# Performance work log

Measured on AMD Instinct MI355X. Metric: run time of the kernel, lower is better.

The kernel has to match this reference:

```python
import jax, jax.numpy as jnp
import numpy as np

L = 2        # layer_depth
H = 128      # rnn_size (== embedding dim)
V = 50257    # vocab_size
B = 100      # batch_size
T = 50       # seq_length


def setup_inputs() -> dict:
    key = jax.random.key(0)
    ks = jax.random.split(key, 8)
    inp = {
        'input_data': jax.random.randint(ks[0], (B, T), 0, V, dtype=jnp.int32),
        # embedding ~ U(-0.08, 0.08) as in the original
        'embedding': jax.random.uniform(ks[1], (V, H), jnp.float32, -0.08, 0.08),
        # per-layer GRU params; input dim == H for every layer
        'gate_k': jax.random.normal(ks[2], (L, 2 * H, 2 * H), jnp.float32) * 0.05,
        'gate_b': jnp.ones((L, 2 * H), jnp.float32),  # TF GRUCell gate bias init = 1.0
        'cand_k': jax.random.normal(ks[3], (L, 2 * H, H), jnp.float32) * 0.05,
        'cand_b': jnp.zeros((L, H), jnp.float32),
        'softmax_w': jax.random.normal(ks[4], (V, H), jnp.float32) * 0.05,
        'softmax_b': jnp.zeros((V,), jnp.float32),
    }
    return inp


def _gru_scan(x_bth, gate_k, gate_b, cand_k, cand_b):
    # x_bth: [B, T, H] embedded inputs. Stacked L-layer GRU, TF GRUCell math:
    #   r,u = sigmoid([x,h] @ Wg + bg);  c = tanh([x, r*h] @ Wc + bc)
    #   h' = u*h + (1-u)*c
    x_tbh = jnp.swapaxes(x_bth, 0, 1)  # [T, B, H]
    h0 = jnp.zeros((L, x_bth.shape[0], H), x_bth.dtype)

    def step(hs, x_t):
        inp = x_t
        new_hs = []
        for l in range(L):
            h = hs[l]
            g = jax.nn.sigmoid(jnp.concatenate([inp, h], -1) @ gate_k[l] + gate_b[l])
            r, u = g[:, :H], g[:, H:]
            c = jnp.tanh(jnp.concatenate([inp, r * h], -1) @ cand_k[l] + cand_b[l])
            h_new = u * h + (1.0 - u) * c
            new_hs.append(h_new)
            inp = h_new
        return jnp.stack(new_hs), inp

    final_state, out_tbh = jax.lax.scan(step, h0, x_tbh)
    return jnp.swapaxes(out_tbh, 0, 1), final_state  # [B, T, H], [L, B, H]


def reference(input_data, embedding, gate_k, gate_b, cand_k, cand_b, softmax_w, softmax_b):
    x = embedding[input_data]                                   # [B, T, H]
    out, _ = _gru_scan(x, gate_k, gate_b, cand_k, cand_b)       # [B, T, H]
    out = out.reshape(-1, H)                                    # [B*T, H]
    logits = out @ softmax_w.T + softmax_b                      # [B*T, V]
    probs = jax.nn.softmax(logits, axis=-1)
    return logits, probs
```

## Files before the change

### kernel.cpp

```cpp
#include <hip/hip_runtime.h>
#include <hip/hip_bf16.h>
#include <math.h>

#define GL 2
#define GH 128
#define GH2 256
#define GV 50257
#define GB 100
#define GT 50
#define GM 5000
#define NT 393
#define MT 40

typedef __attribute__((ext_vector_type(4))) float f32x4;
typedef __attribute__((ext_vector_type(8))) short bf16x8;

__global__ __launch_bounds__(1024) void gru_kernel(
    const int* __restrict__ tok,
    const float* __restrict__ emb,
    const float* __restrict__ gate_k,
    const float* __restrict__ gate_b,
    const float* __restrict__ cand_k,
    const float* __restrict__ cand_b,
    float* __restrict__ out)
{
    const int b = blockIdx.x;
    const int tid = threadIdx.x;

    __shared__ float xin[GH2];
    __shared__ float hs[2][GH];
    __shared__ float g[GH2];
    __shared__ float gpart[4][GH2];
    __shared__ float cpart[8][GH];

    if (tid < GH) { hs[0][tid] = 0.f; hs[1][tid] = 0.f; }
    __syncthreads();

    for (int t = 0; t < GT; ++t) {
        const int token = tok[b * GT + t];
        if (tid < GH) xin[tid] = emb[(size_t)token * GH + tid];

        for (int l = 0; l < GL; ++l) {
            if (tid >= GH && tid < GH2) xin[tid] = hs[l][tid - GH];
            __syncthreads();

            {
                const int j  = tid & 255;
                const int t4 = tid >> 8;
                const float* gcol = gate_k + (size_t)l * GH2 * GH2 + (size_t)(t4 * 64) * GH2 + j;
                const float* xv = xin + t4 * 64;
                float acc = 0.f;
                #pragma unroll 16
                for (int i = 0; i < 64; ++i) acc += xv[i] * gcol[(size_t)i * GH2];
                gpart[t4][j] = acc;
            }
            __syncthreads();
            if (tid < GH2) {
                float s = gpart[0][tid] + gpart[1][tid] + gpart[2][tid] + gpart[3][tid]
                        + gate_b[l * GH2 + tid];
                g[tid] = 1.f / (1.f + expf(-s));
            }
            __syncthreads();
            if (tid >= GH && tid < GH2) xin[tid] = g[tid - GH] * hs[l][tid - GH];
            __syncthreads();

            {
                const int j  = tid & 127;
                const int t8 = tid >> 7;
                const float* ccol = cand_k + (size_t)l * GH2 * GH + (size_t)(t8 * 32) * GH + j;
                const float* xv = xin + t8 * 32;
                float acc = 0.f;
                #pragma unroll 16
                for (int i = 0; i < 32; ++i) acc += xv[i] * ccol[(size_t)i * GH];
                cpart[t8][j] = acc;
            }
            __syncthreads();
            if (tid < GH) {
                float csum = 0.f;
                #pragma unroll
                for (int p = 0; p < 8; ++p) csum += cpart[p][tid];
                const float c = tanhf(csum + cand_b[l * GH + tid]);
                const float u = g[GH + tid];
                const float hn = u * hs[l][tid] + (1.f - u) * c;
                hs[l][tid] = hn;
                xin[tid] = hn;
                if (l == GL - 1) out[(size_t)(b * GT + t) * GH + tid] = hn;
            }
            __syncthreads();
        }
    }
}

__device__ __forceinline__ unsigned short f2bf(float x) {
    union { float f; unsigned u; } c; c.f = x;
    unsigned r = c.u + 0x7FFFu + ((c.u >> 16) & 1u);
    return (unsigned short)(r >> 16);
}
__device__ __forceinline__ float bf2f(unsigned short b) {
    union { unsigned u; float f; } c; c.u = ((unsigned)b) << 16; return c.f;
}

__global__ __launch_bounds__(256) void prep_kernel(
    const float* __restrict__ src, unsigned short* __restrict__ dst,
    int ntiles, int nrows)
{
    const int idx = blockIdx.x * 256 + threadIdx.x;
    if (idx >= ntiles * 4 * 128) return;
    const int r    = idx & 127;
    const int c    = idx >> 7;
    const int cs   = c & 3;
    const int tile = c >> 2;
    int row = tile * 128 + r; if (row > nrows - 1) row = nrows - 1;
    const float* s = src + (size_t)row * GH + (cs & 1) * 64;
    unsigned short* d = dst + (size_t)c * 8192 + r * 64;
    const bool lo = (cs >= 2);
    const int rx = r & 7;

    #pragma unroll
    for (int gq = 0; gq < 8; ++gq) {
        float x[8];
        *(float4*)(x)     = *(const float4*)(s + gq * 8);
        *(float4*)(x + 4) = *(const float4*)(s + gq * 8 + 4);
        unsigned u[4];
        #pragma unroll
        for (int q = 0; q < 4; ++q) {
            const float a0 = x[q * 2], a1 = x[q * 2 + 1];
            const unsigned short hi0 = f2bf(a0), hi1 = f2bf(a1);
            unsigned short h0, h1;
            if (lo) { h0 = f2bf(a0 - bf2f(hi0)); h1 = f2bf(a1 - bf2f(hi1)); }
            else    { h0 = hi0; h1 = hi1; }
            u[q] = (unsigned)h0 | ((unsigned)h1 << 16);
        }
        *(uint4*)(d + (size_t)((gq ^ rx) * 8)) = *(const uint4*)u;
    }
}

__global__ __launch_bounds__(256) void mfma_logits_kernel(
    const unsigned short* __restrict__ Ap, const unsigned short* __restrict__ Wp,
    const float* __restrict__ bias,
    float* __restrict__ logits, float* __restrict__ pmax, float* __restrict__ psum)
{
    __shared__ unsigned short ldsA[8192];
    __shared__ unsigned short ldsW[8192];
    __shared__ float sM[2][128];
    __shared__ float sS[2][128];

    const int bm  = blockIdx.x;
    const int bt  = blockIdx.y;
    const int tid = threadIdx.x;
    const int wid  = tid >> 6;
    const int lane = tid & 63;
    const int wm = wid >> 1, wn = wid & 1;
    const int l15 = lane & 15, l4 = lane >> 4;

    f32x4 acc[4][4];
    #pragma unroll
    for (int i = 0; i < 4; ++i)
        #pragma unroll
        for (int j = 0; j < 4; ++j) acc[i][j] = (f32x4){0.f, 0.f, 0.f, 0.f};

    #pragma unroll
    for (int s = 0; s < 6; ++s) {
        const int ac = (s < 2) ? s : (s < 4) ? (s - 2) : (s - 2);
        const int wc = (s < 4) ? s : (s - 4);
        const unsigned short* ga = Ap + (size_t)(bm * 4 + ac) * 8192 + wid * 2048 + lane * 8;
        const unsigned short* gw = Wp + (size_t)(bt * 4 + wc) * 8192 + wid * 2048 + lane * 8;
        #pragma unroll
        for (int i = 0; i < 4; ++i)
            __builtin_amdgcn_global_load_lds(
                (const __attribute__((address_space(1))) void*)(ga + i * 512),
                (__attribute__((address_space(3))) void*)(&ldsA[wid * 2048 + i * 512]), 16, 0, 0);
        #pragma unroll
        for (int i = 0; i < 4; ++i)
            __builtin_amdgcn_global_load_lds(
                (const __attribute__((address_space(1))) void*)(gw + i * 512),
                (__attribute__((address_space(3))) void*)(&ldsW[wid * 2048 + i * 512]), 16, 0, 0);
        __syncthreads();

        #pragma unroll
        for (int ks = 0; ks < 2; ++ks) {
            bf16x8 af[4], bf[4];
            #pragma unroll
            for (int mi = 0; mi < 4; ++mi) {
                const int row = wm * 64 + mi * 16 + l15;
                const int off = row * 64 + ((ks * 32 + l4 * 8) ^ ((row & 7) << 3));
                af[mi] = *(const bf16x8*)&ldsA[off];
            }
            #pragma unroll
            for (int nj = 0; nj < 4; ++nj) {
                const int row = wn * 64 + nj * 16 + l15;
                const int off = row * 64 + ((ks * 32 + l4 * 8) ^ ((row & 7) << 3));
                bf[nj] = *(const bf16x8*)&ldsW[off];
            }
            #pragma unroll
            for (int mi = 0; mi < 4; ++mi)
                #pragma unroll
                for (int nj = 0; nj < 4; ++nj)
                    acc[mi][nj] = __builtin_amdgcn_mfma_f32_16x16x32_bf16(
                        af[mi], bf[nj], acc[mi][nj], 0, 0, 0);
        }
        __syncthreads();
    }

    float bj[4]; bool nv[4];
    #pragma unroll
    for (int nj = 0; nj < 4; ++nj) {
        const int n = bt * 128 + wn * 64 + nj * 16 + l15;
        nv[nj] = (n < GV);
        bj[nj] = nv[nj] ? bias[n] : 0.f;
    }
    #pragma unroll
    for (int mi = 0; mi < 4; ++mi) {
        #pragma unroll
        for (int r = 0; r < 4; ++r) {
            const int rowb = wm * 64 + mi * 16 + l4 * 4 + r;
            const int m = bm * 128 + rowb;
            float v[4];
            #pragma unroll
            for (int nj = 0; nj < 4; ++nj) v[nj] = acc[mi][nj][r] + bj[nj];
            if (m < GM) {
                #pragma unroll
                for (int nj = 0; nj < 4; ++nj)
                    if (nv[nj])
                        logits[(size_t)m * GV + (bt * 128 + wn * 64 + nj * 16 + l15)] = v[nj];
            }
            float mx = -INFINITY;
            #pragma unroll
            for (int nj = 0; nj < 4; ++nj) if (nv[nj]) mx = fmaxf(mx, v[nj]);
            #pragma unroll
            for (int d = 1; d < 16; d <<= 1) mx = fmaxf(mx, __shfl_xor(mx, d));
            float se = 0.f;
            #pragma unroll
            for (int nj = 0; nj < 4; ++nj) if (nv[nj]) se += __expf(v[nj] - mx);
            #pragma unroll
            for (int d = 1; d < 16; d <<= 1) se += __shfl_xor(se, d);
            if (l15 == 0) { sM[wn][rowb] = mx; sS[wn][rowb] = se; }
        }
    }
    __syncthreads();
    if (tid < 128) {
        const int m = bm * 128 + tid;
        if (m < GM) {
            const float m0 = sM[0][tid], m1 = sM[1][tid];
            const float M = fmaxf(m0, m1);
            const float S = sS[0][tid] * __expf(m0 - M) + sS[1][tid] * __expf(m1 - M);
            pmax[(size_t)m * NT + bt] = M;
            psum[(size_t)m * NT + bt] = S;
        }
    }
}

__global__ __launch_bounds__(64) void reduce_kernel(
    const float* __restrict__ pmax, const float* __restrict__ psum,
    float* __restrict__ rowM, float* __restrict__ rowInvS)
{
    const int m = blockIdx.x;
    const int lane = threadIdx.x;
    float M = -INFINITY, S = 0.f;
    for (int t = lane; t < NT; t += 64) {
        const float m2 = pmax[(size_t)m * NT + t];
        const float s2 = psum[(size_t)m * NT + t];
        const float nM = fmaxf(M, m2);
        S = S * expf(M - nM) + s2 * expf(m2 - nM);
        M = nM;
    }
    #pragma unroll
    for (int d = 1; d < 64; d <<= 1) {
        const float m2 = __shfl_xor(M, d);
        const float s2 = __shfl_xor(S, d);
        const float nM = fmaxf(M, m2);
        S = S * expf(M - nM) + s2 * expf(m2 - nM);
        M = nM;
    }
    if (lane == 0) { rowM[m] = M; rowInvS[m] = 1.f / S; }
}

__global__ __launch_bounds__(256) void probs_kernel(
    const float* __restrict__ logits,
    const float* __restrict__ rowM, const float* __restrict__ rowInvS,
    float* __restrict__ probs)
{
    const float4* L4 = reinterpret_cast<const float4*>(logits);
    float4* P4 = reinterpret_cast<float4*>(probs);
    const int n4 = (int)(((long long)GM * GV) / 4);
    const int stride = gridDim.x * blockDim.x;
    for (int i = blockIdx.x * blockDim.x + threadIdx.x; i < n4; i += stride) {
        const float4 v = L4[i];
        const int base = i * 4;
        const int m0 = base / GV;
        const int m3 = (base + 3) / GV;
        float4 o;
        if (m0 == m3) {
            const float M = rowM[m0], Is = rowInvS[m0];
            o.x = __expf(v.x - M) * Is;
            o.y = __expf(v.y - M) * Is;
            o.z = __expf(v.z - M) * Is;
            o.w = __expf(v.w - M) * Is;
        } else {
            const int ma = base / GV, mb = (base + 1) / GV;
            const int mc = (base + 2) / GV, md = (base + 3) / GV;
            o.x = __expf(v.x - rowM[ma]) * rowInvS[ma];
            o.y = __expf(v.y - rowM[mb]) * rowInvS[mb];
            o.z = __expf(v.z - rowM[mc]) * rowInvS[mc];
            o.w = __expf(v.w - rowM[md]) * rowInvS[md];
        }
        P4[i] = o;
    }
}

extern "C" void kernel_launch(void* const* d_in, const int* in_sizes, int n_in,
                              void* d_out, int out_size, void* d_ws, size_t ws_size,
                              hipStream_t stream) {
    const int*   tok    = (const int*)d_in[0];
    const float* emb    = (const float*)d_in[1];
    const float* gate_k = (const float*)d_in[2];
    const float* gate_b = (const float*)d_in[3];
    const float* cand_k = (const float*)d_in[4];
    const float* cand_b = (const float*)d_in[5];
    const float* W      = (const float*)d_in[6];
    const float* bias   = (const float*)d_in[7];

    float* logits = (float*)d_out;
    float* probs  = logits + (size_t)GM * GV;

    float* ws = (float*)d_ws;
    float* gruout = ws;
    unsigned short* Ap = (unsigned short*)(gruout + 640000);
    unsigned short* Wp = Ap + (size_t)MT * 4 * 8192;
    float* pmax    = (float*)(Wp + (size_t)NT * 4 * 8192);
    float* psum    = pmax + (size_t)GM * NT;
    float* rowM    = psum + (size_t)GM * NT;
    float* rowInvS = rowM + GM;

    gru_kernel<<<GB, 1024, 0, stream>>>(tok, emb, gate_k, gate_b, cand_k, cand_b, gruout);

    prep_kernel<<<(MT * 4 * 128 + 255) / 256, 256, 0, stream>>>(gruout, Ap, MT, GM);
    prep_kernel<<<(NT * 4 * 128 + 255) / 256, 256, 0, stream>>>(W, Wp, NT, GV);

    dim3 g2(MT, NT);
    mfma_logits_kernel<<<g2, 256, 0, stream>>>(Ap, Wp, bias, logits, pmax, psum);

    reduce_kernel<<<GM, 64, 0, stream>>>(pmax, psum, rowM, rowInvS);

    probs_kernel<<<4096, 256, 0, stream>>>(logits, rowM, rowInvS, probs);
}
```

Baseline: 1.369 ms.

## Share each W tile across two M tiles in 512-thread logits blocks

The logits GEMM block now covers 256 rows with 8 waves and two A tiles in LDS that share one W tile, which halves the number of W loads from global memory. The six-stage schedule is rewritten so that A and W chunks are staged separately, and redundant reloads are skipped when a chunk is already resident. The price is more LDS per block, larger blocks and extra barriers. The kernel is likely bound by writing logits, so the gain may be limited.

Measured after the change: 1.363 ms. No clear change (-0.4%).

```diff
diff --git a/kernel.cpp b/kernel.cpp
--- a/kernel.cpp
+++ b/kernel.cpp
@@ -11,6 +11,7 @@
 #define GM 5000
 #define NT 393
 #define MT 40
+#define MT2 20
 
 typedef __attribute__((ext_vector_type(4))) float f32x4;
 typedef __attribute__((ext_vector_type(8))) short bf16x8;
@@ -135,22 +136,24 @@
     }
 }
 
-__global__ __launch_bounds__(256) void mfma_logits_kernel(
+__global__ __launch_bounds__(512, 2) void mfma_logits_kernel(
     const unsigned short* __restrict__ Ap, const unsigned short* __restrict__ Wp,
     const float* __restrict__ bias,
     float* __restrict__ logits, float* __restrict__ pmax, float* __restrict__ psum)
 {
-    __shared__ unsigned short ldsA[8192];
+    __shared__ unsigned short ldsA[2][8192];
     __shared__ unsigned short ldsW[8192];
-    __shared__ float sM[2][128];
-    __shared__ float sS[2][128];
+    __shared__ float sM[2][256];
+    __shared__ float sS[2][256];
 
     const int bm  = blockIdx.x;
     const int bt  = blockIdx.y;
     const int tid = threadIdx.x;
     const int wid  = tid >> 6;
     const int lane = tid & 63;
-    const int wm = wid >> 1, wn = wid & 1;
+    const int mt = wid >> 2;
+    const int wm = (wid >> 1) & 1;
+    const int wn = wid & 1;
     const int l15 = lane & 15, l4 = lane >> 4;
 
     f32x4 acc[4][4];
@@ -159,48 +162,68 @@
         #pragma unroll
         for (int j = 0; j < 4; ++j) acc[i][j] = (f32x4){0.f, 0.f, 0.f, 0.f};
 
-    #pragma unroll
-    for (int s = 0; s < 6; ++s) {
-        const int ac = (s < 2) ? s : (s < 4) ? (s - 2) : (s - 2);
-        const int wc = (s < 4) ? s : (s - 4);
-        const unsigned short* ga = Ap + (size_t)(bm * 4 + ac) * 8192 + wid * 2048 + lane * 8;
-        const unsigned short* gw = Wp + (size_t)(bt * 4 + wc) * 8192 + wid * 2048 + lane * 8;
-        #pragma unroll
-        for (int i = 0; i < 4; ++i)
-            __builtin_amdgcn_global_load_lds(
-                (const __attribute__((address_space(1))) void*)(ga + i * 512),
-                (__attribute__((address_space(3))) void*)(&ldsA[wid * 2048 + i * 512]), 16, 0, 0);
-        #pragma unroll
-        for (int i = 0; i < 4; ++i)
-            __builtin_amdgcn_global_load_lds(
-                (const __attribute__((address_space(1))) void*)(gw + i * 512),
-                (__attribute__((address_space(3))) void*)(&ldsW[wid * 2048 + i * 512]), 16, 0, 0);
-        __syncthreads();
-
-        #pragma unroll
-        for (int ks = 0; ks < 2; ++ks) {
-            bf16x8 af[4], bf[4];
-            #pragma unroll
-            for (int mi = 0; mi < 4; ++mi) {
-                const int row = wm * 64 + mi * 16 + l15;
-                const int off = row * 64 + ((ks * 32 + l4 * 8) ^ ((row & 7) << 3));
-                af[mi] = *(const bf16x8*)&ldsA[off];
-            }
-            #pragma unroll
-            for (int nj = 0; nj < 4; ++nj) {
-                const int row = wn * 64 + nj * 16 + l15;
-                const int off = row * 64 + ((ks * 32 + l4 * 8) ^ ((row & 7) << 3));
-                bf[nj] = *(const bf16x8*)&ldsW[off];
-            }
-            #pragma unroll
-            for (int mi = 0; mi < 4; ++mi)
-                #pragma unroll
-                for (int nj = 0; nj < 4; ++nj)
-                    acc[mi][nj] = __builtin_amdgcn_mfma_f32_16x16x32_bf16(
-                        af[mi], bf[nj], acc[mi][nj], 0, 0, 0);
-        }
-        __syncthreads();
-    }
+#define STAGE_A(MT_, CH)                                                                \
+    {                                                                                   \
+        const unsigned short* g = Ap + (size_t)((bm * 2 + MT_) * 4 + CH) * 8192 + tid * 8; \
+        __builtin_amdgcn_global_load_lds(                                               \
+            (const __attribute__((address_space(1))) void*)(g),                         \
+            (__attribute__((address_space(3))) void*)(&ldsA[MT_][tid * 8]), 16, 0, 0);  \
+        __builtin_amdgcn_global_load_lds(                                               \
+            (const __attribute__((address_space(1))) void*)(g + 4096),                  \
+            (__attribute__((address_space(3))) void*)(&ldsA[MT_][tid * 8 + 4096]), 16, 0, 0); \
+    }
+#define STAGE_W(CH)                                                                     \
+    {                                                                                   \
+        const unsigned short* g = Wp + (size_t)(bt * 4 + CH) * 8192 + tid * 8;          \
+        __builtin_amdgcn_global_load_lds(                                               \
+            (const __attribute__((address_space(1))) void*)(g),                         \
+            (__attribute__((address_space(3))) void*)(&ldsW[tid * 8]), 16, 0, 0);       \
+        __builtin_amdgcn_global_load_lds(                                               \
+            (const __attribute__((address_space(1))) void*)(g + 4096),                  \
+            (__attribute__((address_space(3))) void*)(&ldsW[tid * 8 + 4096]), 16, 0, 0); \
+    }
+#define COMPUTE                                                                         \
+    {                                                                                   \
+        _Pragma("unroll")                                                               \
+        for (int ks = 0; ks < 2; ++ks) {                                                \
+            bf16x8 af[4], bfr[4];                                                       \
+            _Pragma("unroll")                                                           \
+            for (int mi = 0; mi < 4; ++mi) {                                            \
+                const int row = wm * 64 + mi * 16 + l15;                                \
+                const int off = row * 64 + ((ks * 32 + l4 * 8) ^ ((row & 7) << 3));     \
+                af[mi] = *(const bf16x8*)&ldsA[mt][off];                                \
+            }                                                                           \
+            _Pragma("unroll")                                                           \
+            for (int nj = 0; nj < 4; ++nj) {                                            \
+                const int row = wn * 64 + nj * 16 + l15;                                \
+                const int off = row * 64 + ((ks * 32 + l4 * 8) ^ ((row & 7) << 3));     \
+                bfr[nj] = *(const bf16x8*)&ldsW[off];                                   \
+            }                                                                           \
+            _Pragma("unroll")                                                           \
+            for (int mi = 0; mi < 4; ++mi)                                              \
+                _Pragma("unroll")                                                       \
+                for (int nj = 0; nj < 4; ++nj)                                          \
+                    acc[mi][nj] = __builtin_amdgcn_mfma_f32_16x16x32_bf16(              \
+                        af[mi], bfr[nj], acc[mi][nj], 0, 0, 0);                         \
+        }                                                                               \
+    }
+
+    STAGE_A(0, 0); STAGE_A(1, 0); STAGE_W(2);
+    __syncthreads();  COMPUTE;
+    __syncthreads();  STAGE_W(0);
+    __syncthreads();  COMPUTE;
+    __syncthreads();  STAGE_A(0, 2); STAGE_A(1, 2);
+    __syncthreads();  COMPUTE;
+    __syncthreads();  STAGE_A(0, 1); STAGE_A(1, 1); STAGE_W(3);
+    __syncthreads();  COMPUTE;
+    __syncthreads();  STAGE_W(1);
+    __syncthreads();  COMPUTE;
+    __syncthreads();  STAGE_A(0, 3); STAGE_A(1, 3);
+    __syncthreads();  COMPUTE;
+
+#undef STAGE_A
+#undef STAGE_W
+#undef COMPUTE
 
     float bj[4]; bool nv[4];
     #pragma unroll
@@ -213,8 +236,8 @@
     for (int mi = 0; mi < 4; ++mi) {
         #pragma unroll
         for (int r = 0; r < 4; ++r) {
-            const int rowb = wm * 64 + mi * 16 + l4 * 4 + r;
-            const int m = bm * 128 + rowb;
+            const int rowb = mt * 128 + wm * 64 + mi * 16 + l4 * 4 + r;
+            const int m = bm * 256 + rowb;
             float v[4];
             #pragma unroll
             for (int nj = 0; nj < 4; ++nj) v[nj] = acc[mi][nj][r] + bj[nj];
@@ -238,8 +261,8 @@
         }
     }
     __syncthreads();
-    if (tid < 128) {
-        const int m = bm * 128 + tid;
+    if (tid < 256) {
+        const int m = bm * 256 + tid;
         if (m < GM) {
             const float m0 = sM[0][tid], m1 = sM[1][tid];
             const float M = fmaxf(m0, m1);
@@ -337,8 +360,8 @@
     prep_kernel<<<(MT * 4 * 128 + 255) / 256, 256, 0, stream>>>(gruout, Ap, MT, GM);
     prep_kernel<<<(NT * 4 * 128 + 255) / 256, 256, 0, stream>>>(W, Wp, NT, GV);
 
-    dim3 g2(MT, NT);
-    mfma_logits_kernel<<<g2, 256, 0, stream>>>(Ap, Wp, bias, logits, pmax, psum);
+    dim3 g2(MT2, NT);
+    mfma_logits_kernel<<<g2, 512, 0, stream>>>(Ap, Wp, bias, logits, pmax, psum);
 
     reduce_kernel<<<GM, 64, 0, stream>>>(pmax, psum, rowM, rowInvS);
 
```
